# Kernel optimization log

Measured on AMD Instinct MI355X. Metric: run time of the kernel, lower is better.

The kernel has to match this reference:

```python
import jax, jax.numpy as jnp
import numpy as np
import math

C = 128

def setup_inputs() -> dict:
    key = jax.random.key(0)
    ks = jax.random.split(key, 6)
    B, N, M = 4, 8192, 2048
    s = 1.0 / math.sqrt(C)
    return {
        "pcd_up": jax.random.normal(ks[0], (B, C, N), dtype=jnp.float32),
        "pcd_down": jax.random.normal(ks[1], (B, C, M), dtype=jnp.float32),
        "wq": jax.random.normal(ks[2], (C, C), dtype=jnp.float32) * s,
        "wk": jax.random.normal(ks[3], (C, C), dtype=jnp.float32) * s,
        "wv": jax.random.normal(ks[4], (C, C), dtype=jnp.float32) * s,
        "wskip": jax.random.normal(ks[5], (C, C), dtype=jnp.float32) * s,
    }

def reference(pcd_up, pcd_down, wq, wk, wv, wskip):
    # Conv1d(kernel=1, no bias) == per-point linear: w @ x over channel dim
    q = jnp.einsum('oc,bcn->bon', wq, pcd_up)      # [B,C,N]
    k = jnp.einsum('oc,bcm->bom', wk, pcd_down)    # [B,C,M]
    v = jnp.einsum('oc,bcm->bom', wv, pcd_down)    # [B,C,M]
    energy = jnp.einsum('bcn,bcm->bnm', q, k)      # [B,N,M]
    scale = math.sqrt(q.shape[1])                  # sqrt(C): q.shape[-2] in torch
    attn = jax.nn.softmax(energy / scale, axis=-1)
    x = jnp.einsum('bnm,bcm->bcn', attn, v)        # [B,C,N]
    skip = jnp.einsum('oc,bcn->bon', wskip, pcd_up)
    return skip + x
```

## Files before the change

kernel.cpp:

```cpp
#include <hip/hip_runtime.h>
#include <hip/hip_bf16.h>
#include <math.h>

#define C_DIM 128
#define B_DIM 4
#define N_DIM 8192
#define M_DIM 2048
#define NT_KV 32

typedef unsigned short u16;
typedef unsigned int u32;
typedef short bf16x8 __attribute__((ext_vector_type(8)));
typedef float f32x4 __attribute__((ext_vector_type(4)));
typedef float f32x16 __attribute__((ext_vector_type(16)));
typedef u32 u32x4 __attribute__((ext_vector_type(4)));

__device__ inline u16 f2bf(float f) {
  u32 u = __builtin_bit_cast(u32, f);
  u += 0x7fffu + ((u >> 16) & 1u);
  return (u16)(u >> 16);
}
__device__ inline u32 cvtpk_bf16(float lo, float hi) {
  u32 r;
  asm("v_cvt_pk_bf16_f32 %0, %1, %2" : "=v"(r) : "v"(lo), "v"(hi));
  return r;
}

template <int MODE>
__device__ inline void proj_pass(const float* __restrict__ W, float wscale,
                                 const u16* __restrict__ xt_s,
                                 u16* __restrict__ outh,
                                 int b, int X, int x0, int t) {
  const int l = t & 63, w = t >> 6, lr = l & 15, lh = (l >> 4) & 3;
  bf16x8 wf[2][4];
  #pragma unroll
  for (int ot = 0; ot < 2; ++ot)
    #pragma unroll
    for (int kc = 0; kc < 4; ++kc) {
      const float* wp = &W[(size_t)(w * 32 + ot * 16 + lr) * 128 + kc * 32 + lh * 8];
      float4 a0 = *(const float4*)wp;
      float4 a1 = *(const float4*)(wp + 4);
      bf16x8 f;
      f[0] = (short)f2bf(a0.x * wscale); f[1] = (short)f2bf(a0.y * wscale);
      f[2] = (short)f2bf(a0.z * wscale); f[3] = (short)f2bf(a0.w * wscale);
      f[4] = (short)f2bf(a1.x * wscale); f[5] = (short)f2bf(a1.y * wscale);
      f[6] = (short)f2bf(a1.z * wscale); f[7] = (short)f2bf(a1.w * wscale);
      wf[ot][kc] = f;
    }
  f32x4 acc[2][4];
  #pragma unroll
  for (int ot = 0; ot < 2; ++ot)
    #pragma unroll
    for (int xt = 0; xt < 4; ++xt) acc[ot][xt] = 0.f;

  #pragma unroll
  for (int xt = 0; xt < 4; ++xt) {
    int xx = xt * 16 + lr;
    #pragma unroll
    for (int kc = 0; kc < 4; ++kc) {
      bf16x8 bf = *(const bf16x8*)&xt_s[xx * 128 + ((kc * 32 + lh * 8) ^ ((xx & 15) << 3))];
      #pragma unroll
      for (int ot = 0; ot < 2; ++ot)
        acc[ot][xt] = __builtin_amdgcn_mfma_f32_16x16x32_bf16(wf[ot][kc], bf, acc[ot][xt], 0, 0, 0);
    }
  }
  #pragma unroll
  for (int ot = 0; ot < 2; ++ot) {
    int o0 = w * 32 + ot * 16 + lh * 4;
    #pragma unroll
    for (int xt = 0; xt < 4; ++xt) {
      int xg = x0 + xt * 16 + lr;
      if constexpr (MODE == 0) {
        u16 h[4];
        #pragma unroll
        for (int r = 0; r < 4; ++r) h[r] = f2bf(acc[ot][xt][r]);
        *(uint2*)&outh[((size_t)b * X + xg) * 128 + o0] = *(uint2*)h;
      } else if constexpr (MODE == 2) {
        int tt = xg >> 6, mt = (xg >> 5) & 1, ms = xg & 31;
        int kcK = o0 >> 4, lh1p = (o0 >> 3) & 1, e0 = o0 & 7;
        u16 h[4];
        #pragma unroll
        for (int r = 0; r < 4; ++r) h[r] = f2bf(acc[ot][xt][r]);
        size_t off = ((((size_t)(b * NT_KV + tt) * 2 + mt) * 8 + kcK) * 64 + (ms | (lh1p << 5))) * 8 + e0;
        *(uint2*)&outh[off] = *(uint2*)h;
      } else {
        int tt = xg >> 6, sv = (xg >> 4) & 3, lh1m = (xg >> 3) & 1, e = xg & 7;
        int ctv = o0 >> 5;
        #pragma unroll
        for (int r = 0; r < 4; ++r) {
          int cs = (o0 + r) & 31;
          size_t off = ((((size_t)(b * NT_KV + tt) * 4 + ctv) * 4 + sv) * 64 + (cs | (lh1m << 5))) * 8 + e;
          outh[off] = f2bf(acc[ot][xt][r]);
        }
      }
    }
  }
}

template <int MODE_A, int MODE_B>
__global__ __launch_bounds__(256, 2) void proj_kernel(
    const float* __restrict__ in, const float* __restrict__ WA, const float* __restrict__ WB,
    u16* __restrict__ hA, u16* __restrict__ hB, int X, float wscaleA) {
  __shared__ u16 xt_s[64 * 128];
  const int b = blockIdx.y, x0 = blockIdx.x * 64, t = threadIdx.x;
  #pragma unroll
  for (int pp = 0; pp < 8; ++pp) {
    int c = pp * 16 + (t >> 4);
    int x4 = (t & 15) * 4;
    float4 v = *(const float4*)&in[((size_t)b * 128 + c) * X + x0 + x4];
    xt_s[(x4 + 0) * 128 + (c ^ (((x4 + 0) & 15) << 3))] = f2bf(v.x);
    xt_s[(x4 + 1) * 128 + (c ^ (((x4 + 1) & 15) << 3))] = f2bf(v.y);
    xt_s[(x4 + 2) * 128 + (c ^ (((x4 + 2) & 15) << 3))] = f2bf(v.z);
    xt_s[(x4 + 3) * 128 + (c ^ (((x4 + 3) & 15) << 3))] = f2bf(v.w);
  }
  __syncthreads();
  proj_pass<MODE_A>(WA, wscaleA, xt_s, hA, b, X, x0, t);
  if constexpr (MODE_B >= 0)
    proj_pass<MODE_B>(WB, 1.0f, xt_s, hB, b, X, x0, t);
}

__device__ inline void stage_kv(const u16* __restrict__ gK, const u16* __restrict__ gV,
                                u16* lK, u16* lV, int tile, int t) {
  const u16* ks = gK + (size_t)tile * 8192;
  const u16* vs = gV + (size_t)tile * 8192;
  #pragma unroll
  for (int i = 0; i < 2; ++i) {
    int ch = t + i * 512;
    __builtin_amdgcn_global_load_lds((const __attribute__((address_space(1))) void*)(ks + ch * 8),
                                     (__attribute__((address_space(3))) void*)(lK + ch * 8), 16, 0, 0);
    __builtin_amdgcn_global_load_lds((const __attribute__((address_space(1))) void*)(vs + ch * 8),
                                     (__attribute__((address_space(3))) void*)(lV + ch * 8), 16, 0, 0);
  }
}

__global__ __launch_bounds__(512, 2) void attn_kernel(
    const u16* __restrict__ Qt, const u16* __restrict__ Kt2,
    const u16* __restrict__ Vp, const float* __restrict__ up,
    const float* __restrict__ wskip, float* __restrict__ out) {
  __shared__ union {
    u16 kv[2][2][8192];
    float od[4][4096];
  } lds;
  __shared__ float lb[4][64];

  const int bid = blockIdx.x;
  const int xcd = bid & 7, b = xcd & 3, slot = bid >> 3;
  const int n0 = ((xcd >> 2) * 32 + slot) * 128;
  const int t = threadIdx.x, w = t >> 6, l = t & 63, lh1 = l >> 5;
  const int h = w >> 2;
  const int nq = n0 + (w & 3) * 32 + (l & 31);

  bf16x8 qf[8];
  #pragma unroll
  for (int kc = 0; kc < 8; ++kc)
    qf[kc] = *(const bf16x8*)&Qt[((size_t)b * N_DIM + nq) * 128 + kc * 16 + lh1 * 8];

  const u16* gK = Kt2 + (size_t)b * 262144;
  const u16* gV = Vp + (size_t)b * 262144;

  f32x16 acco[4];
  #pragma unroll
  for (int ct = 0; ct < 4; ++ct) acco[ct] = 0.f;
  float lrun = 0.f;

  bf16x8 pf[2];
  bf16x8 vreg[8];
  #pragma unroll
  for (int u = 0; u < 2; ++u) pf[u] = (bf16x8)0;
  #pragma unroll
  for (int x = 0; x < 8; ++x) vreg[x] = (bf16x8)0;

  stage_kv(gK, gV, lds.kv[0][0], lds.kv[0][1], 0, t);
  __syncthreads();

  #pragma unroll 2
  for (int i = 0; i < NT_KV; ++i) {
    const int cur = i & 1;
    if (i + 1 < NT_KV)
      stage_kv(gK, gV, lds.kv[cur ^ 1][0], lds.kv[cur ^ 1][1], i + 1, t);
    const u16* kl = lds.kv[cur][0];
    const u16* vl = lds.kv[cur][1];

    f32x16 sacc = 0.f;
    __builtin_amdgcn_s_setprio(1);
    #pragma unroll
    for (int kc = 0; kc < 8; ++kc) {
      bf16x8 kf = *(const bf16x8*)&kl[((h * 8 + kc) * 64 + l) * 8];
      sacc = __builtin_amdgcn_mfma_f32_32x32x16_bf16(kf, qf[kc], sacc, 0, 0, 0);
    }
    #pragma unroll
    for (int u = 0; u < 2; ++u)
      #pragma unroll
      for (int ct = 0; ct < 4; ++ct)
        acco[ct] = __builtin_amdgcn_mfma_f32_32x32x16_bf16(vreg[ct * 2 + u], pf[u], acco[ct], 0, 0, 0);
    __builtin_amdgcn_s_setprio(0);
    __builtin_amdgcn_sched_barrier(0);

    #pragma unroll
    for (int ct = 0; ct < 4; ++ct)
      #pragma unroll
      for (int u = 0; u < 2; ++u)
        vreg[ct * 2 + u] = *(const bf16x8*)&vl[((ct * 4 + 2 * h + u) * 64 + l) * 8];

    #pragma unroll
    for (int r = 0; r < 16; ++r) sacc[r] = exp2f(sacc[r]);
    {
      float a0 = (sacc[0] + sacc[1]) + (sacc[2] + sacc[3]);
      float a1 = (sacc[4] + sacc[5]) + (sacc[6] + sacc[7]);
      float a2 = (sacc[8] + sacc[9]) + (sacc[10] + sacc[11]);
      float a3 = (sacc[12] + sacc[13]) + (sacc[14] + sacc[15]);
      lrun += (a0 + a1) + (a2 + a3);
    }
    u32 gp[4][2];
    #pragma unroll
    for (int j = 0; j < 4; ++j) {
      gp[j][0] = cvtpk_bf16(sacc[j * 4 + 0], sacc[j * 4 + 1]);
      gp[j][1] = cvtpk_bf16(sacc[j * 4 + 2], sacc[j * 4 + 3]);
    }
    #pragma unroll
    for (int u = 0; u < 2; ++u) {
      u32 a0 = gp[2 * u][0], a1 = gp[2 * u][1];
      u32 b0 = gp[2 * u + 1][0], b1 = gp[2 * u + 1][1];
      asm("v_permlane32_swap_b32 %0, %1" : "+v"(a0), "+v"(b0));
      asm("v_permlane32_swap_b32 %0, %1" : "+v"(a1), "+v"(b1));
      u32x4 fv; fv.x = a0; fv.y = a1; fv.z = b0; fv.w = b1;
      pf[u] = __builtin_bit_cast(bf16x8, fv);
    }
    __syncthreads();
  }

  __builtin_amdgcn_s_setprio(1);
  #pragma unroll
  for (int u = 0; u < 2; ++u)
    #pragma unroll
    for (int ct = 0; ct < 4; ++ct)
      acco[ct] = __builtin_amdgcn_mfma_f32_32x32x16_bf16(vreg[ct * 2 + u], pf[u], acco[ct], 0, 0, 0);
  __builtin_amdgcn_s_setprio(0);

  float lt = lrun + __shfl_xor(lrun, 32, 64);

  if (w >= 4) {
    float* dst = lds.od[w - 4];
    #pragma unroll
    for (int ct = 0; ct < 4; ++ct)
      #pragma unroll
      for (int r = 0; r < 16; ++r) dst[(ct * 16 + r) * 64 + l] = acco[ct][r];
    lb[w - 4][l] = lt;
  }
  __syncthreads();
  if (w < 4) {
    const float* src = lds.od[w];
    #pragma unroll
    for (int ct = 0; ct < 4; ++ct)
      #pragma unroll
      for (int r = 0; r < 16; ++r) acco[ct][r] += src[(ct * 16 + r) * 64 + l];
    lt += lb[w][l];

    float inv = 1.0f / lt;
    #pragma unroll
    for (int ct = 0; ct < 4; ++ct)
      #pragma unroll
      for (int r = 0; r < 16; ++r) acco[ct][r] *= inv;

    const float* upb = up + (size_t)b * 128 * N_DIM;
    #pragma unroll
    for (int kc = 0; kc < 8; ++kc) {
      float uv[8];
      #pragma unroll
      for (int e = 0; e < 8; ++e)
        uv[e] = upb[(size_t)(kc * 16 + lh1 * 8 + e) * N_DIM + nq];
      u32x4 ufv;
      ufv.x = cvtpk_bf16(uv[0], uv[1]);
      ufv.y = cvtpk_bf16(uv[2], uv[3]);
      ufv.z = cvtpk_bf16(uv[4], uv[5]);
      ufv.w = cvtpk_bf16(uv[6], uv[7]);
      bf16x8 upf = __builtin_bit_cast(bf16x8, ufv);
      #pragma unroll
      for (int ct = 0; ct < 4; ++ct) {
        const float* wp = &wskip[(size_t)(ct * 32 + (l & 31)) * 128 + kc * 16 + lh1 * 8];
        float4 w0 = *(const float4*)wp;
        float4 w1 = *(const float4*)(wp + 4);
        u32x4 wfv;
        wfv.x = cvtpk_bf16(w0.x, w0.y);
        wfv.y = cvtpk_bf16(w0.z, w0.w);
        wfv.z = cvtpk_bf16(w1.x, w1.y);
        wfv.w = cvtpk_bf16(w1.z, w1.w);
        bf16x8 wsf = __builtin_bit_cast(bf16x8, wfv);
        acco[ct] = __builtin_amdgcn_mfma_f32_32x32x16_bf16(wsf, upf, acco[ct], 0, 0, 0);
      }
    }

    #pragma unroll
    for (int ct = 0; ct < 4; ++ct)
      #pragma unroll
      for (int r = 0; r < 16; ++r) {
        int c = ct * 32 + (r & 3) + 8 * (r >> 2) + 4 * lh1;
        out[((size_t)b * 128 + c) * N_DIM + nq] = acco[ct][r];
      }
  }
}

extern "C" void kernel_launch(void* const* d_in, const int* in_sizes, int n_in,
                              void* d_out, int out_size, void* d_ws, size_t ws_size,
                              hipStream_t stream) {
  const float* up    = (const float*)d_in[0];
  const float* down  = (const float*)d_in[1];
  const float* wq    = (const float*)d_in[2];
  const float* wk    = (const float*)d_in[3];
  const float* wv    = (const float*)d_in[4];
  const float* wskip = (const float*)d_in[5];
  float* out = (float*)d_out;

  u16* Qt  = (u16*)d_ws;
  u16* Kt2 = Qt + (size_t)B_DIM * N_DIM * C_DIM;
  u16* Vp  = Kt2 + (size_t)B_DIM * M_DIM * C_DIM;

  const float qscale = (float)(1.4426950408889634 / sqrt(128.0));

  hipLaunchKernelGGL((proj_kernel<0, -1>), dim3(N_DIM / 64, B_DIM), dim3(256), 0, stream,
                     up, wq, nullptr, Qt, nullptr, N_DIM, qscale);
  hipLaunchKernelGGL((proj_kernel<2, 3>), dim3(M_DIM / 64, B_DIM), dim3(256), 0, stream,
                     down, wk, wv, Kt2, Vp, M_DIM, 1.0f);
  hipLaunchKernelGGL((attn_kernel), dim3(256), dim3(512), 0, stream,
                     Qt, Kt2, Vp, up, wskip, out);
}
```

Baseline: 74.00 us.

## Double attention block to 1024 threads and split KV across four wave groups

The attention kernel now runs 16 waves per block and stages twice as many keys and values per tile, so each wave group handles a quarter of the key range and the loop runs half as many iterations. The P·V MFMAs are no longer deferred by one iteration with V fragments held in registers. They now read V from LDS right after the softmax in the same iteration. The partial accumulators are combined with a two-level LDS reduction. This lowers iteration and barrier count per block, but it removes the overlap between the two matmuls and raises register pressure under a 1024-thread launch bound.

New measurement: 89.09 us. 1.2x slower.

```diff
diff --git a/kernel.cpp b/kernel.cpp
--- a/kernel.cpp
+++ b/kernel.cpp
@@ -121,11 +121,11 @@
 
 __device__ inline void stage_kv(const u16* __restrict__ gK, const u16* __restrict__ gV,
                                 u16* lK, u16* lV, int tile, int t) {
-  const u16* ks = gK + (size_t)tile * 8192;
-  const u16* vs = gV + (size_t)tile * 8192;
+  const u16* ks = gK + (size_t)tile * 16384;
+  const u16* vs = gV + (size_t)tile * 16384;
   #pragma unroll
   for (int i = 0; i < 2; ++i) {
-    int ch = t + i * 512;
+    int ch = t + i * 1024;
     __builtin_amdgcn_global_load_lds((const __attribute__((address_space(1))) void*)(ks + ch * 8),
                                      (__attribute__((address_space(3))) void*)(lK + ch * 8), 16, 0, 0);
     __builtin_amdgcn_global_load_lds((const __attribute__((address_space(1))) void*)(vs + ch * 8),
@@ -133,15 +133,16 @@
   }
 }
 
-__global__ __launch_bounds__(512, 2) void attn_kernel(
+__global__ __launch_bounds__(1024, 4) void attn_kernel(
     const u16* __restrict__ Qt, const u16* __restrict__ Kt2,
     const u16* __restrict__ Vp, const float* __restrict__ up,
     const float* __restrict__ wskip, float* __restrict__ out) {
   __shared__ union {
-    u16 kv[2][2][8192];
-    float od[4][4096];
+    u16 kv[2][2][16384];
+    float od[8][4096];
   } lds;
-  __shared__ float lb[4][64];
+  __shared__ float lb1[8][64];
+  __shared__ float lb2[4][64];
 
   const int bid = blockIdx.x;
   const int xcd = bid & 7, b = xcd & 3, slot = bid >> 3;
@@ -163,20 +164,12 @@
   for (int ct = 0; ct < 4; ++ct) acco[ct] = 0.f;
   float lrun = 0.f;
 
-  bf16x8 pf[2];
-  bf16x8 vreg[8];
-  #pragma unroll
-  for (int u = 0; u < 2; ++u) pf[u] = (bf16x8)0;
-  #pragma unroll
-  for (int x = 0; x < 8; ++x) vreg[x] = (bf16x8)0;
-
   stage_kv(gK, gV, lds.kv[0][0], lds.kv[0][1], 0, t);
   __syncthreads();
 
-  #pragma unroll 2
-  for (int i = 0; i < NT_KV; ++i) {
+  for (int i = 0; i < 16; ++i) {
     const int cur = i & 1;
-    if (i + 1 < NT_KV)
+    if (i + 1 < 16)
       stage_kv(gK, gV, lds.kv[cur ^ 1][0], lds.kv[cur ^ 1][1], i + 1, t);
     const u16* kl = lds.kv[cur][0];
     const u16* vl = lds.kv[cur][1];
@@ -188,19 +181,7 @@
       bf16x8 kf = *(const bf16x8*)&kl[((h * 8 + kc) * 64 + l) * 8];
       sacc = __builtin_amdgcn_mfma_f32_32x32x16_bf16(kf, qf[kc], sacc, 0, 0, 0);
     }
-    #pragma unroll
-    for (int u = 0; u < 2; ++u)
-      #pragma unroll
-      for (int ct = 0; ct < 4; ++ct)
-        acco[ct] = __builtin_amdgcn_mfma_f32_32x32x16_bf16(vreg[ct * 2 + u], pf[u], acco[ct], 0, 0, 0);
     __builtin_amdgcn_s_setprio(0);
-    __builtin_amdgcn_sched_barrier(0);
-
-    #pragma unroll
-    for (int ct = 0; ct < 4; ++ct)
-      #pragma unroll
-      for (int u = 0; u < 2; ++u)
-        vreg[ct * 2 + u] = *(const bf16x8*)&vl[((ct * 4 + 2 * h + u) * 64 + l) * 8];
 
     #pragma unroll
     for (int r = 0; r < 16; ++r) sacc[r] = exp2f(sacc[r]);
@@ -217,6 +198,7 @@
       gp[j][0] = cvtpk_bf16(sacc[j * 4 + 0], sacc[j * 4 + 1]);
       gp[j][1] = cvtpk_bf16(sacc[j * 4 + 2], sacc[j * 4 + 3]);
     }
+    bf16x8 pf[2];
     #pragma unroll
     for (int u = 0; u < 2; ++u) {
       u32 a0 = gp[2 * u][0], a1 = gp[2 * u][1];
@@ -226,26 +208,47 @@
       u32x4 fv; fv.x = a0; fv.y = a1; fv.z = b0; fv.w = b1;
       pf[u] = __builtin_bit_cast(bf16x8, fv);
     }
+
+    const u16* vq = vl + (size_t)(h >> 1) * 8192;
+    __builtin_amdgcn_s_setprio(1);
+    #pragma unroll
+    for (int u = 0; u < 2; ++u)
+      #pragma unroll
+      for (int ct = 0; ct < 4; ++ct) {
+        bf16x8 vf = *(const bf16x8*)&vq[((ct * 4 + (h & 1) * 2 + u) * 64 + l) * 8];
+        acco[ct] = __builtin_amdgcn_mfma_f32_32x32x16_bf16(vf, pf[u], acco[ct], 0, 0, 0);
+      }
+    __builtin_amdgcn_s_setprio(0);
     __syncthreads();
   }
 
-  __builtin_amdgcn_s_setprio(1);
-  #pragma unroll
-  for (int u = 0; u < 2; ++u)
-    #pragma unroll
-    for (int ct = 0; ct < 4; ++ct)
-      acco[ct] = __builtin_amdgcn_mfma_f32_32x32x16_bf16(vreg[ct * 2 + u], pf[u], acco[ct], 0, 0, 0);
-  __builtin_amdgcn_s_setprio(0);
-
   float lt = lrun + __shfl_xor(lrun, 32, 64);
 
-  if (w >= 4) {
+  if (w >= 8) {
+    float* dst = lds.od[w - 8];
+    #pragma unroll
+    for (int ct = 0; ct < 4; ++ct)
+      #pragma unroll
+      for (int r = 0; r < 16; ++r) dst[(ct * 16 + r) * 64 + l] = acco[ct][r];
+    lb1[w - 8][l] = lt;
+  }
+  __syncthreads();
+  if (w < 8) {
+    const float* src = lds.od[w];
+    #pragma unroll
+    for (int ct = 0; ct < 4; ++ct)
+      #pragma unroll
+      for (int r = 0; r < 16; ++r) acco[ct][r] += src[(ct * 16 + r) * 64 + l];
+    lt += lb1[w][l];
+  }
+  __syncthreads();
+  if (w >= 4 && w < 8) {
     float* dst = lds.od[w - 4];
     #pragma unroll
     for (int ct = 0; ct < 4; ++ct)
       #pragma unroll
       for (int r = 0; r < 16; ++r) dst[(ct * 16 + r) * 64 + l] = acco[ct][r];
-    lb[w - 4][l] = lt;
+    lb2[w - 4][l] = lt;
   }
   __syncthreads();
   if (w < 4) {
@@ -254,7 +257,7 @@
     for (int ct = 0; ct < 4; ++ct)
       #pragma unroll
       for (int r = 0; r < 16; ++r) acco[ct][r] += src[(ct * 16 + r) * 64 + l];
-    lt += lb[w][l];
+    lt += lb2[w][l];
 
     float inv = 1.0f / lt;
     #pragma unroll
@@ -321,6 +324,6 @@
                      up, wq, nullptr, Qt, nullptr, N_DIM, qscale);
   hipLaunchKernelGGL((proj_kernel<2, 3>), dim3(M_DIM / 64, B_DIM), dim3(256), 0, stream,
                      down, wk, wv, Kt2, Vp, M_DIM, 1.0f);
-  hipLaunchKernelGGL((attn_kernel), dim3(256), dim3(512), 0, stream,
+  hipLaunchKernelGGL((attn_kernel), dim3(256), dim3(1024), 0, stream,
                      Qt, Kt2, Vp, up, wskip, out);
 }
```

## Fuse Q projection into attention kernel, removing separate Q projection launch

Applied to the files above, without the earlier changes.

Drops the separate Q projection kernel and its bf16 Q workspace round-trip. The attention kernel now loads its pcd_up slice, projects it with wq via MFMA, and rearranges the accumulators into the Q fragment layout with permlane32 swaps. The first KV tile is staged before this work so the projection can overlap that load. The cost is redundant wq loads and conversions in every block, plus more register pressure in the attention kernel.

New measurement: 90.54 us. 22.4% more time.

```diff
diff --git a/kernel.cpp b/kernel.cpp
--- a/kernel.cpp
+++ b/kernel.cpp
@@ -20,6 +20,9 @@
   u += 0x7fffu + ((u >> 16) & 1u);
   return (u16)(u >> 16);
 }
+__device__ inline u32 packbf(float lo, float hi) {
+  return (u32)f2bf(lo) | ((u32)f2bf(hi) << 16);
+}
 __device__ inline u32 cvtpk_bf16(float lo, float hi) {
   u32 r;
   asm("v_cvt_pk_bf16_f32 %0, %1, %2" : "=v"(r) : "v"(lo), "v"(hi));
@@ -27,7 +30,7 @@
 }
 
 template <int MODE>
-__device__ inline void proj_pass(const float* __restrict__ W, float wscale,
+__device__ inline void proj_pass(const float* __restrict__ W,
                                  const u16* __restrict__ xt_s,
                                  u16* __restrict__ outh,
                                  int b, int X, int x0, int t) {
@@ -41,10 +44,10 @@
       float4 a0 = *(const float4*)wp;
       float4 a1 = *(const float4*)(wp + 4);
       bf16x8 f;
-      f[0] = (short)f2bf(a0.x * wscale); f[1] = (short)f2bf(a0.y * wscale);
-      f[2] = (short)f2bf(a0.z * wscale); f[3] = (short)f2bf(a0.w * wscale);
-      f[4] = (short)f2bf(a1.x * wscale); f[5] = (short)f2bf(a1.y * wscale);
-      f[6] = (short)f2bf(a1.z * wscale); f[7] = (short)f2bf(a1.w * wscale);
+      f[0] = (short)f2bf(a0.x); f[1] = (short)f2bf(a0.y);
+      f[2] = (short)f2bf(a0.z); f[3] = (short)f2bf(a0.w);
+      f[4] = (short)f2bf(a1.x); f[5] = (short)f2bf(a1.y);
+      f[6] = (short)f2bf(a1.z); f[7] = (short)f2bf(a1.w);
       wf[ot][kc] = f;
     }
   f32x4 acc[2][4];
@@ -70,12 +73,7 @@
     #pragma unroll
     for (int xt = 0; xt < 4; ++xt) {
       int xg = x0 + xt * 16 + lr;
-      if constexpr (MODE == 0) {
-        u16 h[4];
-        #pragma unroll
-        for (int r = 0; r < 4; ++r) h[r] = f2bf(acc[ot][xt][r]);
-        *(uint2*)&outh[((size_t)b * X + xg) * 128 + o0] = *(uint2*)h;
-      } else if constexpr (MODE == 2) {
+      if constexpr (MODE == 2) {
         int tt = xg >> 6, mt = (xg >> 5) & 1, ms = xg & 31;
         int kcK = o0 >> 4, lh1p = (o0 >> 3) & 1, e0 = o0 & 7;
         u16 h[4];
@@ -97,26 +95,24 @@
   }
 }
 
-template <int MODE_A, int MODE_B>
-__global__ __launch_bounds__(256, 2) void proj_kernel(
-    const float* __restrict__ in, const float* __restrict__ WA, const float* __restrict__ WB,
-    u16* __restrict__ hA, u16* __restrict__ hB, int X, float wscaleA) {
+__global__ __launch_bounds__(256, 2) void proj_kv(
+    const float* __restrict__ down, const float* __restrict__ wk,
+    const float* __restrict__ wv, u16* __restrict__ Kt2, u16* __restrict__ Vp) {
   __shared__ u16 xt_s[64 * 128];
   const int b = blockIdx.y, x0 = blockIdx.x * 64, t = threadIdx.x;
   #pragma unroll
   for (int pp = 0; pp < 8; ++pp) {
     int c = pp * 16 + (t >> 4);
     int x4 = (t & 15) * 4;
-    float4 v = *(const float4*)&in[((size_t)b * 128 + c) * X + x0 + x4];
+    float4 v = *(const float4*)&down[((size_t)b * 128 + c) * M_DIM + x0 + x4];
     xt_s[(x4 + 0) * 128 + (c ^ (((x4 + 0) & 15) << 3))] = f2bf(v.x);
     xt_s[(x4 + 1) * 128 + (c ^ (((x4 + 1) & 15) << 3))] = f2bf(v.y);
     xt_s[(x4 + 2) * 128 + (c ^ (((x4 + 2) & 15) << 3))] = f2bf(v.z);
     xt_s[(x4 + 3) * 128 + (c ^ (((x4 + 3) & 15) << 3))] = f2bf(v.w);
   }
   __syncthreads();
-  proj_pass<MODE_A>(WA, wscaleA, xt_s, hA, b, X, x0, t);
-  if constexpr (MODE_B >= 0)
-    proj_pass<MODE_B>(WB, 1.0f, xt_s, hB, b, X, x0, t);
+  proj_pass<2>(wk, xt_s, Kt2, b, M_DIM, x0, t);
+  proj_pass<3>(wv, xt_s, Vp, b, M_DIM, x0, t);
 }
 
 __device__ inline void stage_kv(const u16* __restrict__ gK, const u16* __restrict__ gV,
@@ -134,9 +130,9 @@
 }
 
 __global__ __launch_bounds__(512, 2) void attn_kernel(
-    const u16* __restrict__ Qt, const u16* __restrict__ Kt2,
-    const u16* __restrict__ Vp, const float* __restrict__ up,
-    const float* __restrict__ wskip, float* __restrict__ out) {
+    const u16* __restrict__ Kt2, const u16* __restrict__ Vp,
+    const float* __restrict__ up, const float* __restrict__ wq,
+    const float* __restrict__ wskip, float* __restrict__ out, float qscale) {
   __shared__ union {
     u16 kv[2][2][8192];
     float od[4][4096];
@@ -150,14 +146,60 @@
   const int h = w >> 2;
   const int nq = n0 + (w & 3) * 32 + (l & 31);
 
-  bf16x8 qf[8];
-  #pragma unroll
-  for (int kc = 0; kc < 8; ++kc)
-    qf[kc] = *(const bf16x8*)&Qt[((size_t)b * N_DIM + nq) * 128 + kc * 16 + lh1 * 8];
-
   const u16* gK = Kt2 + (size_t)b * 262144;
   const u16* gV = Vp + (size_t)b * 262144;
 
+  stage_kv(gK, gV, lds.kv[0][0], lds.kv[0][1], 0, t);
+
+  const float* upb = up + (size_t)b * 128 * N_DIM;
+  bf16x8 upq[8];
+  #pragma unroll
+  for (int ks = 0; ks < 8; ++ks) {
+    float uv[8];
+    #pragma unroll
+    for (int e = 0; e < 8; ++e)
+      uv[e] = upb[(size_t)(ks * 16 + lh1 * 8 + e) * N_DIM + nq];
+    u32x4 ufv;
+    ufv.x = packbf(uv[0], uv[1]);
+    ufv.y = packbf(uv[2], uv[3]);
+    ufv.z = packbf(uv[4], uv[5]);
+    ufv.w = packbf(uv[6], uv[7]);
+    upq[ks] = __builtin_bit_cast(bf16x8, ufv);
+  }
+  bf16x8 qf[8];
+  #pragma unroll
+  for (int cb = 0; cb < 4; ++cb) {
+    f32x16 dacc = 0.f;
+    #pragma unroll
+    for (int ks = 0; ks < 8; ++ks) {
+      const float* wp = &wq[(size_t)(cb * 32 + (l & 31)) * 128 + ks * 16 + lh1 * 8];
+      float4 w0 = *(const float4*)wp;
+      float4 w1 = *(const float4*)(wp + 4);
+      u32x4 wfv;
+      wfv.x = packbf(w0.x * qscale, w0.y * qscale);
+      wfv.y = packbf(w0.z * qscale, w0.w * qscale);
+      wfv.z = packbf(w1.x * qscale, w1.y * qscale);
+      wfv.w = packbf(w1.z * qscale, w1.w * qscale);
+      bf16x8 wqf = __builtin_bit_cast(bf16x8, wfv);
+      dacc = __builtin_amdgcn_mfma_f32_32x32x16_bf16(wqf, upq[ks], dacc, 0, 0, 0);
+    }
+    u32 gp[4][2];
+    #pragma unroll
+    for (int j = 0; j < 4; ++j) {
+      gp[j][0] = packbf(dacc[j * 4 + 0], dacc[j * 4 + 1]);
+      gp[j][1] = packbf(dacc[j * 4 + 2], dacc[j * 4 + 3]);
+    }
+    #pragma unroll
+    for (int u = 0; u < 2; ++u) {
+      u32 a0 = gp[2 * u][0], a1 = gp[2 * u][1];
+      u32 b0 = gp[2 * u + 1][0], b1 = gp[2 * u + 1][1];
+      asm("v_permlane32_swap_b32 %0, %1" : "+v"(a0), "+v"(b0));
+      asm("v_permlane32_swap_b32 %0, %1" : "+v"(a1), "+v"(b1));
+      u32x4 fv; fv.x = a0; fv.y = a1; fv.z = b0; fv.w = b1;
+      qf[cb * 2 + u] = __builtin_bit_cast(bf16x8, fv);
+    }
+  }
+
   f32x16 acco[4];
   #pragma unroll
   for (int ct = 0; ct < 4; ++ct) acco[ct] = 0.f;
@@ -170,7 +212,6 @@
   #pragma unroll
   for (int x = 0; x < 8; ++x) vreg[x] = (bf16x8)0;
 
-  stage_kv(gK, gV, lds.kv[0][0], lds.kv[0][1], 0, t);
   __syncthreads();
 
   #pragma unroll 2
@@ -262,7 +303,6 @@
       #pragma unroll
       for (int r = 0; r < 16; ++r) acco[ct][r] *= inv;
 
-    const float* upb = up + (size_t)b * 128 * N_DIM;
     #pragma unroll
     for (int kc = 0; kc < 8; ++kc) {
       float uv[8];
@@ -311,16 +351,13 @@
   const float* wskip = (const float*)d_in[5];
   float* out = (float*)d_out;
 
-  u16* Qt  = (u16*)d_ws;
-  u16* Kt2 = Qt + (size_t)B_DIM * N_DIM * C_DIM;
+  u16* Kt2 = (u16*)d_ws;
   u16* Vp  = Kt2 + (size_t)B_DIM * M_DIM * C_DIM;
 
   const float qscale = (float)(1.4426950408889634 / sqrt(128.0));
 
-  hipLaunchKernelGGL((proj_kernel<0, -1>), dim3(N_DIM / 64, B_DIM), dim3(256), 0, stream,
-                     up, wq, nullptr, Qt, nullptr, N_DIM, qscale);
-  hipLaunchKernelGGL((proj_kernel<2, 3>), dim3(M_DIM / 64, B_DIM), dim3(256), 0, stream,
-                     down, wk, wv, Kt2, Vp, M_DIM, 1.0f);
+  hipLaunchKernelGGL((proj_kv), dim3(M_DIM / 64, B_DIM), dim3(256), 0, stream,
+                     down, wk, wv, Kt2, Vp);
   hipLaunchKernelGGL((attn_kernel), dim3(256), dim3(512), 0, stream,
-                     Qt, Kt2, Vp, up, wskip, out);
-}
+                     Kt2, Vp, up, wq, wskip, out, qscale);
+}
```
